# Kernel tuning notes

Hardware: AMD Instinct MI355X
Metric: run time of the kernel (lower is better)

## Reference

```python
import jax, jax.numpy as jnp
import numpy as np

N_GENES = 20000
UNITS = 10000
DEG = 32
BATCH = 128

def setup_inputs() -> dict:
    key = jax.random.key(0)
    k1, k2, k3, k4 = jax.random.split(key, 4)
    feature = jax.random.normal(k1, (BATCH, N_GENES), dtype=jnp.float32)
    ppi = jax.random.randint(k2, (UNITS, DEG), 0, N_GENES, dtype=jnp.int64)
    kernel = jax.random.normal(k3, (UNITS,), dtype=jnp.float32)
    bias = jax.random.normal(k4, (UNITS,), dtype=jnp.float32)
    return {"feature": feature, "ppi": ppi, "kernel": kernel, "bias": bias}

def reference(feature, ppi, kernel, bias):
    # gather along gene axis: [B, UNITS, DEG]
    h = jnp.abs(feature[:, ppi])
    # sum over neighbors -> [B, UNITS]
    h = jnp.sum(h, axis=-1)
    h = h * kernel + bias
    return jnp.tanh(h)
```

## Files before the change

kernel.cpp:

```cpp
#include <hip/hip_runtime.h>
#include <hip/hip_fp16.h>
#include <math.h>

#define N_GENES 20000
#define UNITS   10000
#define DEG     32
#define BATCH   128


__global__ __launch_bounds__(256) void transpose_abs_f16_kernel(
    const float* __restrict__ in, __half* __restrict__ out)
{
    __shared__ float tile[32][33];
    const int g0 = blockIdx.x * 32;
    const int b0 = blockIdx.y * 32;
    const int tx = threadIdx.x;
    const int ty = threadIdx.y;
#pragma unroll
    for (int i = 0; i < 32; i += 8)
        tile[ty + i][tx] = fabsf(in[(size_t)(b0 + ty + i) * N_GENES + (g0 + tx)]);
    __syncthreads();
    const int b  = b0 + tx;
    const int p  = b >> 6;
    const int bh = b & 63;
#pragma unroll
    for (int i = 0; i < 32; i += 8) {
        const int g = g0 + ty + i;
        out[((size_t)p * N_GENES + g) * 64 + bh] = __float2half(tile[tx][ty + i]);
    }
}

__global__ __launch_bounds__(256) void gather_unit_v3(
    const __half2* __restrict__ featT,
    const int*   __restrict__ ppi,
    const float* __restrict__ kernelw,
    const float* __restrict__ bias,
    float*       __restrict__ out)
{
    __shared__ int idx[8 * DEG];
    const int tid = threadIdx.x;
    const int u0  = blockIdx.x * 8;

    idx[tid] = ppi[(size_t)u0 * DEG + tid];
    __syncthreads();

    const int lane = tid & 63;
    const int w    = tid >> 6;
    const int dpar = lane >> 5;
    const int ul   = w * 2 + ((lane >> 4) & 1);
    const int bq   = lane & 15;
    const int u    = u0 + ul;
    const float kk = kernelw[u];
    const float cc = bias[u];
    const int* myidx = idx + ul * DEG;

#pragma unroll
    for (int p = 0; p < 2; ++p) {
        const uint2* fp = reinterpret_cast<const uint2*>(featT) + (size_t)p * N_GENES * 16;
        float acc0 = 0.f, acc1 = 0.f, acc2 = 0.f, acc3 = 0.f;
#pragma unroll
        for (int t = 0; t < 16; ++t) {
            const int d = 2 * t + dpar;
            const int g = myidx[d];
            const uint2 raw = fp[(size_t)g * 16 + bq];
            const float2 f0 = __half22float2(*reinterpret_cast<const __half2*>(&raw.x));
            const float2 f1 = __half22float2(*reinterpret_cast<const __half2*>(&raw.y));
            acc0 += f0.x; acc1 += f0.y; acc2 += f1.x; acc3 += f1.y;
        }
        acc0 += __shfl_xor(acc0, 32, 64);
        acc1 += __shfl_xor(acc1, 32, 64);
        acc2 += __shfl_xor(acc2, 32, 64);
        acc3 += __shfl_xor(acc3, 32, 64);

        if (dpar == 0) {
            const int bbase = p * 64 + bq * 4;
            const float h0 = acc0 * kk + cc;
            const float h1 = acc1 * kk + cc;
            const float h2 = acc2 * kk + cc;
            const float h3 = acc3 * kk + cc;
            out[(size_t)(bbase + 0) * UNITS + u] = 1.f - 2.f / (__expf(2.f * h0) + 1.f);
            out[(size_t)(bbase + 1) * UNITS + u] = 1.f - 2.f / (__expf(2.f * h1) + 1.f);
            out[(size_t)(bbase + 2) * UNITS + u] = 1.f - 2.f / (__expf(2.f * h2) + 1.f);
            out[(size_t)(bbase + 3) * UNITS + u] = 1.f - 2.f / (__expf(2.f * h3) + 1.f);
        }
    }
}

extern "C" void kernel_launch(void* const* d_in, const int* in_sizes, int n_in,
                              void* d_out, int out_size, void* d_ws, size_t ws_size,
                              hipStream_t stream) {
    const float* feature = (const float*)d_in[0];
    const int*   ppi     = (const int*)d_in[1];
    const float* kernelw = (const float*)d_in[2];
    const float* bias    = (const float*)d_in[3];
    float* out   = (float*)d_out;
    __half* featT = (__half*)d_ws;

    dim3 g1(N_GENES / 32, BATCH / 32);
    dim3 b1(32, 8);
    transpose_abs_f16_kernel<<<g1, b1, 0, stream>>>(feature, featT);

    gather_unit_v3<<<UNITS / 8, 256, 0, stream>>>(
        (const __half2*)featT, ppi, kernelw, bias, out);
}
```

Baseline: 78.57 us.

## Use full-batch gene rows with 16-byte gathers and staged coalesced output

The transposed feature layout changes from two 64-batch planes to one 128-wide fp16 row per gene, so each lane loads a uint4 (8 batches) and each 16-lane group covers all batches of one neighbor row with a single 256-byte read. Each block now processes 16 units and loops over all 32 neighbors per lane, which removes the cross-half shuffle reduction. Results are staged in shared memory and written as float4 rows, replacing scattered 4-byte stores with a UNITS stride. The trade-offs are more registers per thread, half as many blocks, and an extra barrier.

```diff
diff --git a/kernel.cpp b/kernel.cpp
--- a/kernel.cpp
+++ b/kernel.cpp
@@ -6,7 +6,6 @@
 #define UNITS   10000
 #define DEG     32
 #define BATCH   128
-
 
 __global__ __launch_bounds__(256) void transpose_abs_f16_kernel(
     const float* __restrict__ in, __half* __restrict__ out)
@@ -20,69 +19,68 @@
     for (int i = 0; i < 32; i += 8)
         tile[ty + i][tx] = fabsf(in[(size_t)(b0 + ty + i) * N_GENES + (g0 + tx)]);
     __syncthreads();
-    const int b  = b0 + tx;
-    const int p  = b >> 6;
-    const int bh = b & 63;
 #pragma unroll
-    for (int i = 0; i < 32; i += 8) {
-        const int g = g0 + ty + i;
-        out[((size_t)p * N_GENES + g) * 64 + bh] = __float2half(tile[tx][ty + i]);
-    }
+    for (int i = 0; i < 32; i += 8)
+        out[(size_t)(g0 + ty + i) * BATCH + (b0 + tx)] = __float2half(tile[tx][ty + i]);
 }
 
-__global__ __launch_bounds__(256) void gather_unit_v3(
-    const __half2* __restrict__ featT,
+__global__ __launch_bounds__(256) void gather_unit_v4(
+    const uint4* __restrict__ featT,
     const int*   __restrict__ ppi,
     const float* __restrict__ kernelw,
     const float* __restrict__ bias,
     float*       __restrict__ out)
 {
-    __shared__ int idx[8 * DEG];
+    __shared__ int   idx[16 * DEG];
+    __shared__ float outs[BATCH][20];
     const int tid = threadIdx.x;
-    const int u0  = blockIdx.x * 8;
+    const int u0  = blockIdx.x * 16;
 
-    idx[tid] = ppi[(size_t)u0 * DEG + tid];
+    idx[tid]       = ppi[(size_t)u0 * DEG + tid];
+    idx[tid + 256] = ppi[(size_t)u0 * DEG + tid + 256];
     __syncthreads();
 
     const int lane = tid & 63;
     const int w    = tid >> 6;
-    const int dpar = lane >> 5;
-    const int ul   = w * 2 + ((lane >> 4) & 1);
+    const int ul   = w * 4 + (lane >> 4);
     const int bq   = lane & 15;
-    const int u    = u0 + ul;
+    const int* myidx = idx + ul * DEG;
+
+    float acc0 = 0.f, acc1 = 0.f, acc2 = 0.f, acc3 = 0.f;
+    float acc4 = 0.f, acc5 = 0.f, acc6 = 0.f, acc7 = 0.f;
+
+#pragma unroll 8
+    for (int d = 0; d < DEG; ++d) {
+        const int g = myidx[d];
+        const uint4 raw = featT[(size_t)g * 16 + bq];
+        const float2 f0 = __half22float2(*reinterpret_cast<const __half2*>(&raw.x));
+        const float2 f1 = __half22float2(*reinterpret_cast<const __half2*>(&raw.y));
+        const float2 f2 = __half22float2(*reinterpret_cast<const __half2*>(&raw.z));
+        const float2 f3 = __half22float2(*reinterpret_cast<const __half2*>(&raw.w));
+        acc0 += f0.x; acc1 += f0.y; acc2 += f1.x; acc3 += f1.y;
+        acc4 += f2.x; acc5 += f2.y; acc6 += f3.x; acc7 += f3.y;
+    }
+
+    const int u  = u0 + ul;
     const float kk = kernelw[u];
     const float cc = bias[u];
-    const int* myidx = idx + ul * DEG;
+    const int bb = bq * 8;
 
+    float a[8] = {acc0, acc1, acc2, acc3, acc4, acc5, acc6, acc7};
+#pragma unroll
+    for (int j = 0; j < 8; ++j) {
+        const float h = a[j] * kk + cc;
+        outs[bb + j][ul] = 1.f - 2.f / (__expf(2.f * h) + 1.f);
+    }
+    __syncthreads();
+
+    const int uq   = tid & 3;
+    const int brow = tid >> 2;
 #pragma unroll
     for (int p = 0; p < 2; ++p) {
-        const uint2* fp = reinterpret_cast<const uint2*>(featT) + (size_t)p * N_GENES * 16;
-        float acc0 = 0.f, acc1 = 0.f, acc2 = 0.f, acc3 = 0.f;
-#pragma unroll
-        for (int t = 0; t < 16; ++t) {
-            const int d = 2 * t + dpar;
-            const int g = myidx[d];
-            const uint2 raw = fp[(size_t)g * 16 + bq];
-            const float2 f0 = __half22float2(*reinterpret_cast<const __half2*>(&raw.x));
-            const float2 f1 = __half22float2(*reinterpret_cast<const __half2*>(&raw.y));
-            acc0 += f0.x; acc1 += f0.y; acc2 += f1.x; acc3 += f1.y;
-        }
-        acc0 += __shfl_xor(acc0, 32, 64);
-        acc1 += __shfl_xor(acc1, 32, 64);
-        acc2 += __shfl_xor(acc2, 32, 64);
-        acc3 += __shfl_xor(acc3, 32, 64);
-
-        if (dpar == 0) {
-            const int bbase = p * 64 + bq * 4;
-            const float h0 = acc0 * kk + cc;
-            const float h1 = acc1 * kk + cc;
-            const float h2 = acc2 * kk + cc;
-            const float h3 = acc3 * kk + cc;
-            out[(size_t)(bbase + 0) * UNITS + u] = 1.f - 2.f / (__expf(2.f * h0) + 1.f);
-            out[(size_t)(bbase + 1) * UNITS + u] = 1.f - 2.f / (__expf(2.f * h1) + 1.f);
-            out[(size_t)(bbase + 2) * UNITS + u] = 1.f - 2.f / (__expf(2.f * h2) + 1.f);
-            out[(size_t)(bbase + 3) * UNITS + u] = 1.f - 2.f / (__expf(2.f * h3) + 1.f);
-        }
+        const int b = p * 64 + brow;
+        const float4 v = *reinterpret_cast<const float4*>(&outs[b][uq * 4]);
+        *reinterpret_cast<float4*>(out + (size_t)b * UNITS + u0 + uq * 4) = v;
     }
 }
 
@@ -100,6 +98,6 @@
     dim3 b1(32, 8);
     transpose_abs_f16_kernel<<<g1, b1, 0, stream>>>(feature, featT);
 
-    gather_unit_v3<<<UNITS / 8, 256, 0, stream>>>(
-        (const __half2*)featT, ppi, kernelw, bias, out);
+    gather_unit_v4<<<UNITS / 16, 256, 0, stream>>>(
+        (const uint4*)featT, ppi, kernelw, bias, out);
 }
```

Measured after the change: 78.72 us (median of 2 runs). No clear change (+0.2%).
